# Kernel optimization log

Measured on AMD Instinct MI355X. Metric: run time of the kernel, lower is better.

The kernel has to match this reference:

```python
import jax, jax.numpy as jnp
import numpy as np

# Config (BERT-base with T5-style shared relative attention bias)
B, S, D, H, F, V, L = 16, 512, 768, 12, 3072, 30522, 12
DH = D // H
MAXREL = 128  # bias table has 2*MAXREL+1 = 257 buckets
EPS = 1e-12


def layer_norm(x, w, b):
    mu = jnp.mean(x, axis=-1, keepdims=True)
    var = jnp.mean(jnp.square(x - mu), axis=-1, keepdims=True)
    return (x - mu) * jax.lax.rsqrt(var + EPS) * w + b


def setup_inputs() -> dict:
    key = jax.random.key(0)
    ks = jax.random.split(key, 16)
    s = 0.02
    inp = {
        "input_ids": jax.random.randint(ks[0], (B, S), 0, V),
        "attention_mask": jnp.ones((B, S), jnp.float32),
        "word_emb": jax.random.normal(ks[1], (V, D), jnp.float32) * s,
        "pos_emb": jax.random.normal(ks[2], (S, D), jnp.float32) * s,
        "emb_ln_w": jnp.ones((D,), jnp.float32),
        "emb_ln_b": jnp.zeros((D,), jnp.float32),
        "rel_bias_table": jax.random.normal(ks[3], (2 * MAXREL + 1, H), jnp.float32) * s,
        "Wq": jax.random.normal(ks[4], (L, D, D), jnp.float32) * s,
        "bq": jnp.zeros((L, D), jnp.float32),
        "Wk": jax.random.normal(ks[5], (L, D, D), jnp.float32) * s,
        "bk": jnp.zeros((L, D), jnp.float32),
        "Wv": jax.random.normal(ks[6], (L, D, D), jnp.float32) * s,
        "bv": jnp.zeros((L, D), jnp.float32),
        "Wo": jax.random.normal(ks[7], (L, D, D), jnp.float32) * s,
        "bo": jnp.zeros((L, D), jnp.float32),
        "attn_ln_w": jnp.ones((L, D), jnp.float32),
        "attn_ln_b": jnp.zeros((L, D), jnp.float32),
        "Wi": jax.random.normal(ks[8], (L, F, D), jnp.float32) * s,
        "bi": jnp.zeros((L, F), jnp.float32),
        "Wd": jax.random.normal(ks[9], (L, D, F), jnp.float32) * s,
        "bd": jnp.zeros((L, D), jnp.float32),
        "out_ln_w": jnp.ones((L, D), jnp.float32),
        "out_ln_b": jnp.zeros((L, D), jnp.float32),
    }
    return inp


def _encoder(input_ids, attention_mask, word_emb, pos_emb, emb_ln_w, emb_ln_b,
             rel_bias_table, Wq, bq, Wk, bk, Wv, bv, Wo, bo, attn_ln_w, attn_ln_b,
             Wi, bi, Wd, bd, out_ln_w, out_ln_b):
    b, s = input_ids.shape
    # Embeddings: word + learned absolute position, then LayerNorm
    h = word_emb[input_ids] + pos_emb[:s][None, :, :]
    h = layer_norm(h, emb_ln_w, emb_ln_b)

    # Shared relative position bias: [H, S, S]
    pos = jnp.arange(s)
    rel = jnp.clip(pos[None, :] - pos[:, None], -MAXREL, MAXREL) + MAXREL
    rel_bias = jnp.transpose(rel_bias_table[rel], (2, 0, 1))[None]  # [1,H,S,S]

    # Additive attention mask: [B,1,1,S]
    add_mask = (1.0 - attention_mask)[:, None, None, :] * -10000.0
    scale = 1.0 / np.sqrt(DH)

    def step(h, p):
        wq, bq_, wk, bk_, wv, bv_, wo, bo_, lw1, lb1, wi, bi_, wd, bd_, lw2, lb2 = p
        q = (h @ wq.T + bq_).reshape(b, s, H, DH)
        k = (h @ wk.T + bk_).reshape(b, s, H, DH)
        v = (h @ wv.T + bv_).reshape(b, s, H, DH)
        scores = jnp.einsum('bqhd,bkhd->bhqk', q, k) * scale + rel_bias + add_mask
        attn = jax.nn.softmax(scores, axis=-1)
        ctx = jnp.einsum('bhqk,bkhd->bqhd', attn, v).reshape(b, s, D)
        h1 = layer_norm(h + (ctx @ wo.T + bo_), lw1, lb1)
        inter = jax.nn.gelu(h1 @ wi.T + bi_, approximate=False)
        h2 = layer_norm(h1 + (inter @ wd.T + bd_), lw2, lb2)
        return h2, None

    params = (Wq, bq, Wk, bk, Wv, bv, Wo, bo, attn_ln_w, attn_ln_b,
              Wi, bi, Wd, bd, out_ln_w, out_ln_b)
    h, _ = jax.lax.scan(step, h, params)
    return h


def reference(input_ids, attention_mask, word_emb, pos_emb, emb_ln_w, emb_ln_b,
              rel_bias_table, Wq, bq, Wk, bk, Wv, bv, Wo, bo, attn_ln_w, attn_ln_b,
              Wi, bi, Wd, bd, out_ln_w, out_ln_b):
    return _encoder(input_ids, attention_mask, word_emb, pos_emb, emb_ln_w, emb_ln_b,
                    rel_bias_table, Wq, bq, Wk, bk, Wv, bv, Wo, bo, attn_ln_w, attn_ln_b,
                    Wi, bi, Wd, bd, out_ln_w, out_ln_b)
```

## Files before the change

### kernel.cpp

```cpp
#include <hip/hip_runtime.h>
#include <cstdint>
#include <cstddef>

#define BB 16
#define SS 512
#define DD 768
#define HH 12
#define FF 3072
#define LL 12
#define DHD 64
#define MM (BB*SS)

typedef __attribute__((ext_vector_type(8))) short bf16x8;
typedef __attribute__((ext_vector_type(4))) float f32x4;

__device__ __forceinline__ ushort f2bf(float f) {
  union { float f; uint32_t u; } x; x.f = f;
  uint32_t r = x.u + 0x7FFFu + ((x.u >> 16) & 1u);
  return (ushort)(r >> 16);
}

__device__ __forceinline__ void glds16(const ushort* g, ushort* l) {
  __builtin_amdgcn_global_load_lds((__attribute__((address_space(1))) void*)g,
                                   (__attribute__((address_space(3))) void*)l,
                                   16, 0, 0);
}

__device__ __forceinline__ float gelu_t(float v) {
  float y = 0.7978845608f * (v + 0.044715f * v * v * v);
  y = fminf(fmaxf(y, -15.f), 15.f);
  float e = __expf(2.f * y);
  return 0.5f * v * (2.f - 2.f / (e + 1.f));
}

__global__ __launch_bounds__(256)
void convw6(const float* __restrict__ s0, const float* __restrict__ s1,
            const float* __restrict__ s2, const float* __restrict__ s3,
            const float* __restrict__ s4, const float* __restrict__ s5,
            ushort* __restrict__ dA, ushort* __restrict__ dB, int perD, int perF)
{
  const int y = blockIdx.y;
  const int per = (y < 4) ? perD : perF;
  const int i = (blockIdx.x * 256 + threadIdx.x) * 4;
  if (i >= per) return;
  const float* s = y == 0 ? s0 : y == 1 ? s1 : y == 2 ? s2 : y == 3 ? s3 : y == 4 ? s4 : s5;
  ushort* dst = (y < 4) ? (dA + (size_t)y * perD) : (dB + (size_t)(y - 4) * perF);
  const float4 v = *(const float4*)(s + i);
  ushort4 o;
  o.x = f2bf(v.x); o.y = f2bf(v.y); o.z = f2bf(v.z); o.w = f2bf(v.w);
  *(ushort4*)(dst + i) = o;
}

__global__ __launch_bounds__(256)
void embed_ln_kernel(const int* __restrict__ ids, const float* __restrict__ wemb,
                     const float* __restrict__ pemb, const float* __restrict__ g,
                     const float* __restrict__ bt, float* __restrict__ hf,
                     ushort* __restrict__ hb)
{
  const int row = blockIdx.x;
  const int s = row & (SS - 1);
  const int id = ids[row];
  const float* wp = wemb + (size_t)id * DD;
  const float* pp = pemb + (size_t)s * DD;
  const int tid = threadIdx.x;
  float v[3]; float sum = 0.f, sq = 0.f;
#pragma unroll
  for (int j = 0; j < 3; ++j) {
    int e = tid + j * 256;
    v[j] = wp[e] + pp[e];
    sum += v[j]; sq += v[j] * v[j];
  }
  __shared__ float red[2][4];
#pragma unroll
  for (int off = 32; off >= 1; off >>= 1) { sum += __shfl_xor(sum, off); sq += __shfl_xor(sq, off); }
  const int lane = tid & 63, wid = tid >> 6;
  if (lane == 0) { red[0][wid] = sum; red[1][wid] = sq; }
  __syncthreads();
  sum = red[0][0] + red[0][1] + red[0][2] + red[0][3];
  sq  = red[1][0] + red[1][1] + red[1][2] + red[1][3];
  const float mean = sum * (1.f / DD);
  const float var  = sq  * (1.f / DD) - mean * mean;
  const float rstd = rsqrtf(var + 1e-12f);
  const size_t base = (size_t)row * DD;
#pragma unroll
  for (int j = 0; j < 3; ++j) {
    int e = tid + j * 256;
    float o = (v[j] - mean) * rstd * g[e] + bt[e];
    hf[base + e] = o;
    hb[base + e] = f2bf(o);
  }
}

__global__ __launch_bounds__(256)
void add_ln2_kernel(const float* __restrict__ res, const float* __restrict__ p0,
                    const float* __restrict__ p1, const float* __restrict__ g,
                    const float* __restrict__ bt, float* __restrict__ hf,
                    ushort* __restrict__ hb)
{
  const int row = blockIdx.x;
  const int tid = threadIdx.x;
  const size_t base = (size_t)row * DD;
  float v[3]; float sum = 0.f, sq = 0.f;
#pragma unroll
  for (int j = 0; j < 3; ++j) {
    int e = tid + j * 256;
    v[j] = res[base + e] + p0[base + e] + p1[base + e];
    sum += v[j]; sq += v[j] * v[j];
  }
  __shared__ float red[2][4];
#pragma unroll
  for (int off = 32; off >= 1; off >>= 1) { sum += __shfl_xor(sum, off); sq += __shfl_xor(sq, off); }
  const int lane = tid & 63, wid = tid >> 6;
  if (lane == 0) { red[0][wid] = sum; red[1][wid] = sq; }
  __syncthreads();
  sum = red[0][0] + red[0][1] + red[0][2] + red[0][3];
  sq  = red[1][0] + red[1][1] + red[1][2] + red[1][3];
  const float mean = sum * (1.f / DD);
  const float var  = sq  * (1.f / DD) - mean * mean;
  const float rstd = rsqrtf(var + 1e-12f);
#pragma unroll
  for (int j = 0; j < 3; ++j) {
    int e = tid + j * 256;
    float o = (v[j] - mean) * rstd * g[e] + bt[e];
    hf[base + e] = o;
    hb[base + e] = f2bf(o);
  }
}

template<int EPI, bool TRV>
__global__ __launch_bounds__(256, 3)
void gemm_ker(const ushort* __restrict__ A,
              const ushort* __restrict__ B0, const ushort* __restrict__ B1,
              const ushort* __restrict__ B2,
              const float* __restrict__ bias0, const float* __restrict__ bias1,
              const float* __restrict__ bias2,
              void* __restrict__ C0, void* __restrict__ C1, void* __restrict__ C2,
              int Kdim, int nblk)
{
  __shared__ ushort As[3][128 * 32];
  __shared__ ushort Bs[3][128 * 32];

  int id = blockIdx.y * gridDim.x + blockIdx.x;
  const int chunk = (gridDim.x * gridDim.y) >> 3;
  id = (id & 7) * chunk + (id >> 3);
  const int bm = id & 63;
  const int bnAll = id >> 6;
  const int sub = bnAll / nblk;
  const int bn = bnAll - sub * nblk;

  const ushort* Bw  = sub == 0 ? B0 : (sub == 1 ? B1 : B2);
  const float* bias = sub == 0 ? bias0 : (sub == 1 ? bias1 : bias2);
  const int Ndim = nblk * 128;

  const int tid = threadIdx.x;
  const int l = tid & 63, w = tid >> 6;
  const int wm = w >> 1, wn = w & 1;
  const int fr = l & 15, fg = l >> 4;

  const int srow_in = l >> 2;
  const int gks = ((l & 3) ^ ((l >> 3) & 3)) * 8;
  const ushort* Agl0 = A  + (size_t)(bm * 128 + w * 16 + srow_in) * Kdim + gks;
  const ushort* Agl1 = Agl0 + (size_t)64 * Kdim;
  const ushort* Bgl0 = Bw + (size_t)(bn * 128 + w * 16 + srow_in) * Kdim + gks;
  const ushort* Bgl1 = Bgl0 + (size_t)64 * Kdim;

  auto stage = [&](int b, int kt) {
    const int ko = kt * 32;
    ushort* al = &As[b][w * 64 * 8];
    ushort* bl = &Bs[b][w * 64 * 8];
    glds16(Agl0 + ko, al);
    glds16(Agl1 + ko, al + 256 * 8);
    glds16(Bgl0 + ko, bl);
    glds16(Bgl1 + ko, bl + 256 * 8);
  };

  const int se = (fg ^ ((fr >> 1) & 3)) * 8;

  f32x4 acc[4][4];
#pragma unroll
  for (int i = 0; i < 4; ++i)
#pragma unroll
    for (int j = 0; j < 4; ++j) acc[i][j] = f32x4{0.f, 0.f, 0.f, 0.f};

  stage(0, 0);
  stage(1, 1);
  asm volatile("s_waitcnt vmcnt(4)" ::: "memory");
  asm volatile("s_barrier" ::: "memory");

  const int nk = Kdim >> 5;
  for (int kt = 0; kt < nk; ++kt) {
    const int rb = kt % 3;
    if (kt + 2 < nk) stage((kt + 2) % 3, kt + 2);

    bf16x8 af[4], bfv[4];
#pragma unroll
    for (int i = 0; i < 4; ++i)
      af[i]  = *(const bf16x8*)&As[rb][(wm * 64 + i * 16 + fr) * 32 + se];
#pragma unroll
    for (int j = 0; j < 4; ++j)
      bfv[j] = *(const bf16x8*)&Bs[rb][(wn * 64 + j * 16 + fr) * 32 + se];

    __builtin_amdgcn_s_setprio(1);
#pragma unroll
    for (int i = 0; i < 4; ++i)
#pragma unroll
      for (int j = 0; j < 4; ++j)
        acc[i][j] = __builtin_amdgcn_mfma_f32_16x16x32_bf16(bfv[j], af[i], acc[i][j], 0, 0, 0);
    __builtin_amdgcn_s_setprio(0);

    if (kt + 1 < nk) {
      if (kt + 2 < nk) { asm volatile("s_waitcnt vmcnt(4)" ::: "memory"); }
      else             { asm volatile("s_waitcnt vmcnt(0)" ::: "memory"); }
      asm volatile("s_barrier" ::: "memory");
    }
  }

#pragma unroll
  for (int i = 0; i < 4; ++i) {
    const int row_g = bm * 128 + wm * 64 + i * 16 + fr;
#pragma unroll
    for (int j = 0; j < 4; ++j) {
      const int col = bn * 128 + wn * 64 + j * 16 + fg * 4;
      const float4 bv4 = *(const float4*)&bias[col];
      const float v0 = acc[i][j][0] + bv4.x;
      const float v1 = acc[i][j][1] + bv4.y;
      const float v2 = acc[i][j][2] + bv4.z;
      const float v3 = acc[i][j][3] + bv4.w;
      if (TRV && sub == 2) {
        const int b_ = row_g >> 9, s_ = row_g & 511;
        const int h_ = col >> 6, d0 = col & 63;
        ushort* vp = (ushort*)C2 + (((size_t)(b_ * HH + h_) * DHD + d0) * SS + s_);
        vp[0] = f2bf(v0); vp[SS] = f2bf(v1); vp[2 * SS] = f2bf(v2); vp[3 * SS] = f2bf(v3);
      } else if (EPI == 2) {
        ushort4 o4;
        o4.x = f2bf(gelu_t(v0)); o4.y = f2bf(gelu_t(v1));
        o4.z = f2bf(gelu_t(v2)); o4.w = f2bf(gelu_t(v3));
        *(ushort4*)&((ushort*)C0)[(size_t)row_g * Ndim + col] = o4;
      } else {
        void* Cout = sub == 0 ? C0 : (sub == 1 ? C1 : C2);
        ushort4 o4;
        o4.x = f2bf(v0); o4.y = f2bf(v1); o4.z = f2bf(v2); o4.w = f2bf(v3);
        *(ushort4*)&((ushort*)Cout)[(size_t)row_g * Ndim + col] = o4;
      }
    }
  }
}

__global__ __launch_bounds__(256, 3)
void gemm_sk(const ushort* __restrict__ A, const ushort* __restrict__ Bw,
             const float* __restrict__ bias, float* __restrict__ P0,
             float* __restrict__ P1, int Kdim)
{
  __shared__ ushort As[3][128 * 32];
  __shared__ ushort Bs[3][128 * 32];

  int id = blockIdx.y * gridDim.x + blockIdx.x;
  const int chunk = (gridDim.x * gridDim.y) >> 3;
  id = (id & 7) * chunk + (id >> 3);
  const int bm = id & 63;
  const int rest = id >> 6;
  const int bn = rest >> 1;
  const int sk = rest & 1;

  const int Kh = Kdim >> 1;

  const int tid = threadIdx.x;
  const int l = tid & 63, w = tid >> 6;
  const int wm = w >> 1, wn = w & 1;
  const int fr = l & 15, fg = l >> 4;

  const int srow_in = l >> 2;
  const int gks = ((l & 3) ^ ((l >> 3) & 3)) * 8;
  const ushort* Agl0 = A  + (size_t)(bm * 128 + w * 16 + srow_in) * Kdim + sk * Kh + gks;
  const ushort* Agl1 = Agl0 + (size_t)64 * Kdim;
  const ushort* Bgl0 = Bw + (size_t)(bn * 128 + w * 16 + srow_in) * Kdim + sk * Kh + gks;
  const ushort* Bgl1 = Bgl0 + (size_t)64 * Kdim;

  auto stage = [&](int b, int kt) {
    const int ko = kt * 32;
    ushort* al = &As[b][w * 64 * 8];
    ushort* bl = &Bs[b][w * 64 * 8];
    glds16(Agl0 + ko, al);
    glds16(Agl1 + ko, al + 256 * 8);
    glds16(Bgl0 + ko, bl);
    glds16(Bgl1 + ko, bl + 256 * 8);
  };

  const int se = (fg ^ ((fr >> 1) & 3)) * 8;

  f32x4 acc[4][4];
#pragma unroll
  for (int i = 0; i < 4; ++i)
#pragma unroll
    for (int j = 0; j < 4; ++j) acc[i][j] = f32x4{0.f, 0.f, 0.f, 0.f};

  stage(0, 0);
  stage(1, 1);
  asm volatile("s_waitcnt vmcnt(4)" ::: "memory");
  asm volatile("s_barrier" ::: "memory");

  const int nk = Kh >> 5;
  for (int kt = 0; kt < nk; ++kt) {
    const int rb = kt % 3;
    if (kt + 2 < nk) stage((kt + 2) % 3, kt + 2);

    bf16x8 af[4], bfv[4];
#pragma unroll
    for (int i = 0; i < 4; ++i)
      af[i]  = *(const bf16x8*)&As[rb][(wm * 64 + i * 16 + fr) * 32 + se];
#pragma unroll
    for (int j = 0; j < 4; ++j)
      bfv[j] = *(const bf16x8*)&Bs[rb][(wn * 64 + j * 16 + fr) * 32 + se];

    __builtin_amdgcn_s_setprio(1);
#pragma unroll
    for (int i = 0; i < 4; ++i)
#pragma unroll
      for (int j = 0; j < 4; ++j)
        acc[i][j] = __builtin_amdgcn_mfma_f32_16x16x32_bf16(bfv[j], af[i], acc[i][j], 0, 0, 0);
    __builtin_amdgcn_s_setprio(0);

    if (kt + 1 < nk) {
      if (kt + 2 < nk) { asm volatile("s_waitcnt vmcnt(4)" ::: "memory"); }
      else             { asm volatile("s_waitcnt vmcnt(0)" ::: "memory"); }
      asm volatile("s_barrier" ::: "memory");
    }
  }

  float* P = sk ? P1 : P0;
  const float bs = sk ? 0.f : 1.f;
#pragma unroll
  for (int i = 0; i < 4; ++i) {
    const int row_g = bm * 128 + wm * 64 + i * 16 + fr;
#pragma unroll
    for (int j = 0; j < 4; ++j) {
      const int col = bn * 128 + wn * 64 + j * 16 + fg * 4;
      const float4 bv4 = *(const float4*)&bias[col];
      float4 o4;
      o4.x = acc[i][j][0] + bv4.x * bs;
      o4.y = acc[i][j][1] + bv4.y * bs;
      o4.z = acc[i][j][2] + bv4.z * bs;
      o4.w = acc[i][j][3] + bv4.w * bs;
      *(float4*)&P[(size_t)row_g * DD + col] = o4;
    }
  }
}

__global__ __launch_bounds__(256, 3)
void attn_kernel(const ushort* __restrict__ qb, const ushort* __restrict__ kb,
                 const ushort* __restrict__ vt, const float* __restrict__ relt,
                 const float* __restrict__ amask, ushort* __restrict__ ctxb)
{
  __shared__ ushort Kt[128][72];
  __shared__ ushort Vt[64][136];
  __shared__ ushort Pl[64][136];
  __shared__ float am_lds[512];
  __shared__ float rel_lds[1024];

  const int tid = threadIdx.x, lane = tid & 63, w = tid >> 6;

  int lin = blockIdx.y * gridDim.x + blockIdx.x;
  lin = (lin & 7) * 192 + (lin >> 3);
  const int qt = lin & 7;
  const int bh = lin >> 3;
  const int b = bh / HH, h = bh - b * HH;
  const int fr = lane & 15, fg = lane >> 4;

  for (int i = tid; i < 512; i += 256)
    am_lds[i] = (1.0f - amask[b * SS + i]) * -10000.0f;
  for (int i = tid; i < 1024; i += 256) {
    int d = i - 512;
    d = min(128, max(-128, d));
    rel_lds[i] = relt[(d + 128) * HH + h];
  }

  bf16x8 qf[2];
  {
    const int qrow = qt * 64 + w * 16 + fr;
    const ushort* p = qb + ((size_t)(b * SS + qrow) * DD) + h * DHD + fg * 8;
    qf[0] = *(const bf16x8*)p;
    qf[1] = *(const bf16x8*)(p + 32);
  }

  f32x4 o[4];
  float mrow[4], lrow[4];
#pragma unroll
  for (int r = 0; r < 4; ++r) { mrow[r] = -1e30f; lrow[r] = 0.f; }
#pragma unroll
  for (int d = 0; d < 4; ++d) o[d] = f32x4{0.f, 0.f, 0.f, 0.f};

  const int skr = tid >> 1;
  const int shd = (tid & 1) * 32;
  const int vrow = tid >> 2;
  const int vcg  = (tid & 3) * 32;
  const ushort* vgl = vt + ((size_t)bh * DHD + vrow) * SS + vcg;

  const int qg0 = qt * 64 + w * 16;

  for (int kt = 0; kt < 4; ++kt) {
    const size_t gbase = ((size_t)(b * SS + kt * 128 + skr) * DD) + h * DHD + shd;
    int4 kr0 = *(const int4*)(kb + gbase);
    int4 kr1 = *(const int4*)(kb + gbase + 8);
    int4 kr2 = *(const int4*)(kb + gbase + 16);
    int4 kr3 = *(const int4*)(kb + gbase + 24);
    const ushort* vp = vgl + kt * 128;
    int4 vr0 = *(const int4*)(vp);
    int4 vr1 = *(const int4*)(vp + 8);
    int4 vr2 = *(const int4*)(vp + 16);
    int4 vr3 = *(const int4*)(vp + 24);

    __syncthreads();
    *(int4*)&Kt[skr][shd]      = kr0;
    *(int4*)&Kt[skr][shd + 8]  = kr1;
    *(int4*)&Kt[skr][shd + 16] = kr2;
    *(int4*)&Kt[skr][shd + 24] = kr3;
    *(int4*)&Vt[vrow][vcg]      = vr0;
    *(int4*)&Vt[vrow][vcg + 8]  = vr1;
    *(int4*)&Vt[vrow][vcg + 16] = vr2;
    *(int4*)&Vt[vrow][vcg + 24] = vr3;
    __syncthreads();

    float sv[8][4];
    __builtin_amdgcn_s_setprio(1);
#pragma unroll
    for (int kc = 0; kc < 8; ++kc) {
      f32x4 s = f32x4{0.f, 0.f, 0.f, 0.f};
      bf16x8 kf0 = *(const bf16x8*)&Kt[kc * 16 + fr][fg * 8];
      bf16x8 kf1 = *(const bf16x8*)&Kt[kc * 16 + fr][32 + fg * 8];
      s = __builtin_amdgcn_mfma_f32_16x16x32_bf16(qf[0], kf0, s, 0, 0, 0);
      s = __builtin_amdgcn_mfma_f32_16x16x32_bf16(qf[1], kf1, s, 0, 0, 0);
      const int col = kt * 128 + kc * 16 + fr;
      const float am = am_lds[col];
      const int ridx = col - qg0 - fg * 4 + 512;
#pragma unroll
      for (int r = 0; r < 4; ++r)
        sv[kc][r] = s[r] * 0.125f + rel_lds[ridx - r] + am;
    }
    __builtin_amdgcn_s_setprio(0);

    float ef[4];
#pragma unroll
    for (int r = 0; r < 4; ++r) {
      float tmax = sv[0][r];
#pragma unroll
      for (int kc = 1; kc < 8; ++kc) tmax = fmaxf(tmax, sv[kc][r]);
#pragma unroll
      for (int off = 1; off < 16; off <<= 1) tmax = fmaxf(tmax, __shfl_xor(tmax, off));
      const float mnew = fmaxf(mrow[r], tmax);
      ef[r] = __expf(mrow[r] - mnew);
      float psum = 0.f;
      const int prow = w * 16 + fg * 4 + r;
#pragma unroll
      for (int kc = 0; kc < 8; ++kc) {
        float p = __expf(sv[kc][r] - mnew);
        psum += p;
        Pl[prow][kc * 16 + fr] = f2bf(p);
      }
#pragma unroll
      for (int off = 1; off < 16; off <<= 1) psum += __shfl_xor(psum, off);
      lrow[r] = lrow[r] * ef[r] + psum;
      mrow[r] = mnew;
    }
#pragma unroll
    for (int dc = 0; dc < 4; ++dc)
#pragma unroll
      for (int r = 0; r < 4; ++r) o[dc][r] *= ef[r];
    __syncthreads();

    __builtin_amdgcn_s_setprio(1);
#pragma unroll
    for (int dc = 0; dc < 4; ++dc)
#pragma unroll
      for (int ks = 0; ks < 4; ++ks) {
        bf16x8 pf = *(const bf16x8*)&Pl[w * 16 + fr][ks * 32 + fg * 8];
        bf16x8 vf = *(const bf16x8*)&Vt[dc * 16 + fr][ks * 32 + fg * 8];
        o[dc] = __builtin_amdgcn_mfma_f32_16x16x32_bf16(pf, vf, o[dc], 0, 0, 0);
      }
    __builtin_amdgcn_s_setprio(0);
  }

#pragma unroll
  for (int dc = 0; dc < 4; ++dc)
#pragma unroll
    for (int r = 0; r < 4; ++r) {
      const int qg = qt * 64 + w * 16 + fg * 4 + r;
      const float v = o[dc][r] / lrow[r];
      ctxb[((size_t)(b * SS + qg) * DD) + h * DHD + dc * 16 + fr] = f2bf(v);
    }
}

extern "C" void kernel_launch(void* const* d_in, const int* in_sizes, int n_in,
                              void* d_out, int out_size, void* d_ws, size_t ws_size,
                              hipStream_t stream) {
  const int*   ids   = (const int*)d_in[0];
  const float* amask = (const float*)d_in[1];
  const float* wemb  = (const float*)d_in[2];
  const float* pemb  = (const float*)d_in[3];
  const float* eln_w = (const float*)d_in[4];
  const float* eln_b = (const float*)d_in[5];
  const float* relt  = (const float*)d_in[6];
  const float* Wq    = (const float*)d_in[7];
  const float* bq    = (const float*)d_in[8];
  const float* Wk    = (const float*)d_in[9];
  const float* bk    = (const float*)d_in[10];
  const float* Wv    = (const float*)d_in[11];
  const float* bv    = (const float*)d_in[12];
  const float* Wo    = (const float*)d_in[13];
  const float* bo    = (const float*)d_in[14];
  const float* aln_w = (const float*)d_in[15];
  const float* aln_b = (const float*)d_in[16];
  const float* Wi    = (const float*)d_in[17];
  const float* bi    = (const float*)d_in[18];
  const float* Wd    = (const float*)d_in[19];
  const float* bd    = (const float*)d_in[20];
  const float* oln_w = (const float*)d_in[21];
  const float* oln_b = (const float*)d_in[22];

  size_t off = 0;
  auto carve = [&](size_t bytes) -> void* {
    void* r = (char*)d_ws + off;
    off += (bytes + 255) & ~(size_t)255;
    return r;
  };
  float*  hf     = (float*) carve((size_t)MM * DD * 4);
  ushort* hb     = (ushort*)carve((size_t)MM * DD * 2);
  ushort* qbuf   = (ushort*)carve((size_t)MM * DD * 2);
  ushort* kbuf   = (ushort*)carve((size_t)MM * DD * 2);
  ushort* vbuf   = (ushort*)carve((size_t)MM * DD * 2);
  ushort* ctxb   = (ushort*)carve((size_t)MM * DD * 2);
  float*  gout   = (float*) carve((size_t)MM * DD * 4);
  float*  gout2  = (float*) carve((size_t)MM * DD * 4);
  ushort* interb = (ushort*)carve((size_t)MM * FF * 2);
  const int PD = DD * DD;
  const int PF = FF * DD;
  ushort* wBded  = (ushort*)carve((size_t)2 * PF * 2);

  ushort* wA = interb;

  embed_ln_kernel<<<MM, 256, 0, stream>>>(ids, wemb, pemb, eln_w, eln_b, hf, hb);

  const dim3 gQKV(MM / 128, 3 * (DD / 128));
  const dim3 gSK(MM / 128, 2 * (DD / 128));
  const dim3 gF(MM / 128, FF / 128);
  const dim3 gA(SS / 64, BB * HH);
  const dim3 gC(PF / 1024, 6);

  for (int l = 0; l < LL; ++l) {
    const size_t wo  = (size_t)l * PD;
    const size_t wio = (size_t)l * PF;

    convw6<<<gC, 256, 0, stream>>>(Wq + wo, Wk + wo, Wv + wo, Wo + wo,
                                   Wi + wio, Wd + wio, wA, wBded, PD, PF);

    gemm_ker<0, true><<<gQKV, 256, 0, stream>>>(hb, wA, wA + PD, wA + 2 * PD,
                                                bq + l * DD, bk + l * DD, bv + l * DD,
                                                qbuf, kbuf, vbuf, DD, DD / 128);

    attn_kernel<<<gA, 256, 0, stream>>>(qbuf, kbuf, vbuf, relt, amask, ctxb);

    gemm_sk<<<gSK, 256, 0, stream>>>(ctxb, wA + 3 * PD, bo + l * DD, gout, gout2, DD);
    add_ln2_kernel<<<MM, 256, 0, stream>>>(hf, gout, gout2,
                                           aln_w + l * DD, aln_b + l * DD, hf, hb);

    gemm_ker<2, false><<<gF, 256, 0, stream>>>(hb, wBded, wBded, wBded,
                                               bi + l * FF, bi + l * FF, bi + l * FF,
                                               interb, interb, interb, DD, FF / 128);
    gemm_sk<<<gSK, 256, 0, stream>>>(interb, wBded + PF, bd + l * DD, gout, gout2, FF);

    float* outp = (l == LL - 1) ? (float*)d_out : hf;
    add_ln2_kernel<<<MM, 256, 0, stream>>>(hf, gout, gout2,
                                           oln_w + l * DD, oln_b + l * DD, outp, hb);
  }
}
```

Baseline: 3.632 ms.

## Switch GEMM kernels from triple to double LDS buffering with higher occupancy

Both GEMM kernels drop from three LDS stages to two, cutting shared memory per block from 48KB to 32KB and raising the launch-bounds occupancy hint from 3 to 4 blocks per CU. The hand-written vmcnt waits and raw barriers are replaced by a plain __syncthreads at the end of each k-step. The goal is more resident blocks to hide latency, but only one tile is prefetched ahead. __syncthreads also waits for all outstanding global-to-LDS loads each iteration, so load latency is less overlapped with MFMA work, and the tighter register budget may cause spills.

```diff
diff --git a/kernel.cpp b/kernel.cpp
--- a/kernel.cpp
+++ b/kernel.cpp
@@ -128,7 +128,7 @@
 }
 
 template<int EPI, bool TRV>
-__global__ __launch_bounds__(256, 3)
+__global__ __launch_bounds__(256, 4)
 void gemm_ker(const ushort* __restrict__ A,
               const ushort* __restrict__ B0, const ushort* __restrict__ B1,
               const ushort* __restrict__ B2,
@@ -137,8 +137,8 @@
               void* __restrict__ C0, void* __restrict__ C1, void* __restrict__ C2,
               int Kdim, int nblk)
 {
-  __shared__ ushort As[3][128 * 32];
-  __shared__ ushort Bs[3][128 * 32];
+  __shared__ ushort As[2][128 * 32];
+  __shared__ ushort Bs[2][128 * 32];
 
   int id = blockIdx.y * gridDim.x + blockIdx.x;
   const int chunk = (gridDim.x * gridDim.y) >> 3;
@@ -183,22 +183,20 @@
     for (int j = 0; j < 4; ++j) acc[i][j] = f32x4{0.f, 0.f, 0.f, 0.f};
 
   stage(0, 0);
-  stage(1, 1);
-  asm volatile("s_waitcnt vmcnt(4)" ::: "memory");
-  asm volatile("s_barrier" ::: "memory");
+  __syncthreads();
 
   const int nk = Kdim >> 5;
+  int cur = 0;
   for (int kt = 0; kt < nk; ++kt) {
-    const int rb = kt % 3;
-    if (kt + 2 < nk) stage((kt + 2) % 3, kt + 2);
+    if (kt + 1 < nk) stage(cur ^ 1, kt + 1);
 
     bf16x8 af[4], bfv[4];
 #pragma unroll
     for (int i = 0; i < 4; ++i)
-      af[i]  = *(const bf16x8*)&As[rb][(wm * 64 + i * 16 + fr) * 32 + se];
+      af[i]  = *(const bf16x8*)&As[cur][(wm * 64 + i * 16 + fr) * 32 + se];
 #pragma unroll
     for (int j = 0; j < 4; ++j)
-      bfv[j] = *(const bf16x8*)&Bs[rb][(wn * 64 + j * 16 + fr) * 32 + se];
+      bfv[j] = *(const bf16x8*)&Bs[cur][(wn * 64 + j * 16 + fr) * 32 + se];
 
     __builtin_amdgcn_s_setprio(1);
 #pragma unroll
@@ -208,11 +206,8 @@
         acc[i][j] = __builtin_amdgcn_mfma_f32_16x16x32_bf16(bfv[j], af[i], acc[i][j], 0, 0, 0);
     __builtin_amdgcn_s_setprio(0);
 
-    if (kt + 1 < nk) {
-      if (kt + 2 < nk) { asm volatile("s_waitcnt vmcnt(4)" ::: "memory"); }
-      else             { asm volatile("s_waitcnt vmcnt(0)" ::: "memory"); }
-      asm volatile("s_barrier" ::: "memory");
-    }
+    __syncthreads();
+    cur ^= 1;
   }
 
 #pragma unroll
@@ -246,13 +241,13 @@
   }
 }
 
-__global__ __launch_bounds__(256, 3)
+__global__ __launch_bounds__(256, 4)
 void gemm_sk(const ushort* __restrict__ A, const ushort* __restrict__ Bw,
              const float* __restrict__ bias, float* __restrict__ P0,
              float* __restrict__ P1, int Kdim)
 {
-  __shared__ ushort As[3][128 * 32];
-  __shared__ ushort Bs[3][128 * 32];
+  __shared__ ushort As[2][128 * 32];
+  __shared__ ushort Bs[2][128 * 32];
 
   int id = blockIdx.y * gridDim.x + blockIdx.x;
   const int chunk = (gridDim.x * gridDim.y) >> 3;
@@ -295,22 +290,20 @@
     for (int j = 0; j < 4; ++j) acc[i][j] = f32x4{0.f, 0.f, 0.f, 0.f};
 
   stage(0, 0);
-  stage(1, 1);
-  asm volatile("s_waitcnt vmcnt(4)" ::: "memory");
-  asm volatile("s_barrier" ::: "memory");
+  __syncthreads();
 
   const int nk = Kh >> 5;
+  int cur = 0;
   for (int kt = 0; kt < nk; ++kt) {
-    const int rb = kt % 3;
-    if (kt + 2 < nk) stage((kt + 2) % 3, kt + 2);
+    if (kt + 1 < nk) stage(cur ^ 1, kt + 1);
 
     bf16x8 af[4], bfv[4];
 #pragma unroll
     for (int i = 0; i < 4; ++i)
-      af[i]  = *(const bf16x8*)&As[rb][(wm * 64 + i * 16 + fr) * 32 + se];
+      af[i]  = *(const bf16x8*)&As[cur][(wm * 64 + i * 16 + fr) * 32 + se];
 #pragma unroll
     for (int j = 0; j < 4; ++j)
-      bfv[j] = *(const bf16x8*)&Bs[rb][(wn * 64 + j * 16 + fr) * 32 + se];
+      bfv[j] = *(const bf16x8*)&Bs[cur][(wn * 64 + j * 16 + fr) * 32 + se];
 
     __builtin_amdgcn_s_setprio(1);
 #pragma unroll
@@ -320,11 +313,8 @@
         acc[i][j] = __builtin_amdgcn_mfma_f32_16x16x32_bf16(bfv[j], af[i], acc[i][j], 0, 0, 0);
     __builtin_amdgcn_s_setprio(0);
 
-    if (kt + 1 < nk) {
-      if (kt + 2 < nk) { asm volatile("s_waitcnt vmcnt(4)" ::: "memory"); }
-      else             { asm volatile("s_waitcnt vmcnt(0)" ::: "memory"); }
-      asm volatile("s_barrier" ::: "memory");
-    }
+    __syncthreads();
+    cur ^= 1;
   }
 
   float* P = sk ? P1 : P0;
```

Result: no change. 3.600 ms (-0.9%).
